# Optimization experiments

Hardware: AMD Instinct MI355X
Metric: run time of the kernel (lower is better)

## Reference

```python
import jax, jax.numpy as jnp
import numpy as np

N = 1000      # dataset / batch samples
D = 2000      # descriptors (e.g., pairwise distances)
A = 200       # atoms
K = 2         # atoms involved per descriptor (distance -> 2)
# nnz = N * D * K * 3 = 12M sparse entries of d_desc/d_pos


def setup_inputs() -> dict:
    key = jax.random.key(0)
    k_val, k_x = jax.random.split(key)
    rng = np.random.default_rng(0)

    # each descriptor involves K atoms (fixed per descriptor, as for distances)
    atoms = rng.integers(0, A, size=(D, K)).astype(np.int32)        # [D, K]

    # expand to per-(sample, descriptor, atom, dim) nonzero entries
    dims = np.arange(3, dtype=np.int32)
    # desc index per nnz within one sample: [D, K, 3] -> flat
    desc_per_sample = np.broadcast_to(np.arange(D, dtype=np.int32)[:, None, None], (D, K, 3)).ravel()
    atom_per_sample = np.broadcast_to(atoms[:, :, None], (D, K, 3)).ravel()
    dim_per_sample = np.broadcast_to(dims[None, None, :], (D, K, 3)).ravel()
    per_sample = D * K * 3

    batch_idx = np.repeat(np.arange(N, dtype=np.int32), per_sample)          # [nnz]
    desc_idx = np.tile(desc_per_sample, N)                                   # [nnz]
    scatter_idx = (batch_idx.astype(np.int64) * (A * 3)
                   + np.tile(atom_per_sample, N).astype(np.int64) * 3
                   + np.tile(dim_per_sample, N)).astype(np.int32)            # [nnz] in [0, N*A*3)

    nnz = N * per_sample
    values = jax.random.normal(k_val, (nnz,), dtype=jnp.float32)             # nonzero d_desc/d_pos
    x = jax.random.normal(k_x, (N, D), dtype=jnp.float32)                    # d_out/d_desc (right input)

    return {
        "values": values,
        "x": x,
        "batch_idx": jnp.asarray(batch_idx),
        "desc_idx": jnp.asarray(desc_idx),
        "scatter_idx": jnp.asarray(scatter_idx),
        "n_atoms": A,
    }


def reference(values, x, batch_idx, desc_idx, scatter_idx, n_atoms):
    # gather right-input entries per nonzero of the sparse left matrix
    right = x[batch_idx, desc_idx]                 # [nnz]
    # per-entry contribution (atom contribution via one descriptor, one dim)
    contrib = right * values                       # [nnz]
    # scatter-add to global d_out/d_pos of shape [N, n_atoms, 3]
    n = x.shape[0]
    out = jax.ops.segment_sum(contrib, scatter_idx, num_segments=n * n_atoms * 3)
    return out.reshape(n, n_atoms, 3)
```

## Files before the change

kernel.cpp:

```cpp
#include <hip/hip_runtime.h>

constexpr int N_SAMPLES  = 1000;
constexpr int D_DESC     = 2000;
constexpr int N_ATOMS    = 200;
constexpr int PER_SAMPLE = 12000;
constexpr int OUT_PER    = 600;
constexpr int N_ENTRIES  = 4000;
constexpr int NH         = 2;
constexpr int EPH        = N_ENTRIES / NH;
constexpr int VPH        = 3 * EPH;
constexpr int XPH        = D_DESC / NH;
constexpr int ELLW_H     = 40;
constexpr int LSENT      = EPH;
constexpr int MTHREADS   = 256;
constexpr int NBLK       = N_SAMPLES * NH;
constexpr int OUT_FLOATS = N_SAMPLES * OUT_PER;
constexpr int OUT_QUADS  = OUT_FLOATS / 4;
constexpr int ZBLKS      = (OUT_QUADS + 255) / 256;
constexpr int ELL_INTS   = NH * N_ATOMS * ELLW_H;
constexpr size_t ELL_BYTES  = (size_t)ELL_INTS * 4;
constexpr size_t PART_BYTES = (size_t)NBLK * OUT_PER * 4;

using f32x4 = __attribute__((ext_vector_type(4))) float;

#define GLD4(dst, ptr) asm volatile("global_load_dwordx4 %0, %1, off" \
    : "=v"(dst) : "v"((unsigned long long)(uintptr_t)(ptr)))

__global__ __launch_bounds__(512)
void setup_kernel(const int* __restrict__ scatter_idx,
                  int* __restrict__ ell,
                  float* __restrict__ out, int zero_out) {
    const int tid = threadIdx.x;
    if (blockIdx.x >= 2) {
        const int i = (blockIdx.x - 2) * 512 + tid;
        if (zero_out && i < OUT_QUADS)
            reinterpret_cast<float4*>(out)[i] = float4{0.f, 0.f, 0.f, 0.f};
        return;
    }
    const int h = blockIdx.x;
    __shared__ int fill[N_ATOMS];
    if (tid < N_ATOMS) fill[tid] = 0;

    int4* ell4 = reinterpret_cast<int4*>(ell + h * N_ATOMS * ELLW_H);
    const int4 sent4 = int4{LSENT, LSENT, LSENT, LSENT};
    for (int i = tid; i < N_ATOMS * ELLW_H / 4; i += 512) ell4[i] = sent4;

    int av[4];
    #pragma unroll
    for (int k = 0; k < 4; ++k) {
        const int le = tid + 512 * k;
        av[k] = (le < EPH) ? (scatter_idx[3 * (h * EPH + le)] / 3) : -1;
    }
    __syncthreads();
    int* ellh = ell + h * N_ATOMS * ELLW_H;
    #pragma unroll
    for (int k = 0; k < 4; ++k) {
        const int le = tid + 512 * k;
        if (av[k] >= 0) {
            const int idx = atomicAdd(&fill[av[k]], 1);
            if (idx < ELLW_H) ellh[av[k] * ELLW_H + idx] = le;
        }
    }
}

template <int MODE>
__global__ __launch_bounds__(MTHREADS)
void SmartDerivatives_kernel(const float* __restrict__ values,
                             const float* __restrict__ x,
                             const int*   __restrict__ ell,
                             float*       __restrict__ pbuf,
                             float*       __restrict__ out) {
    __shared__ __align__(16) float vls[VPH + 4];
    __shared__ __align__(16) float xls[XPH + 4];
    const int bid  = blockIdx.x;
    const int n    = bid >> 1;
    const int h    = bid & 1;
    const int tid  = threadIdx.x;

    const float4* __restrict__ vq = reinterpret_cast<const float4*>(
        values + (size_t)n * PER_SAMPLE + h * VPH);
    const float4* __restrict__ xq = reinterpret_cast<const float4*>(
        x + (size_t)n * D_DESC + h * XPH);

    const int a = (tid < N_ATOMS) ? tid : 0;
    const int4* __restrict__ er =
        reinterpret_cast<const int4*>(ell + ((size_t)h * N_ATOMS + a) * ELLW_H);
    const int4 e0 = er[0], e1 = er[1], e2 = er[2], e3 = er[3], e4 = er[4];

    const int q5 = (tid + 1280 < VPH / 4) ? tid + 1280 : VPH / 4 - 1;
    const int qx = (tid < XPH / 4) ? tid : XPH / 4 - 1;
    f32x4 r0, r1, r2, r3, r4, r5, r6;
    GLD4(r0, vq + tid);
    GLD4(r1, vq + tid + 256);
    GLD4(r2, vq + tid + 512);
    GLD4(r3, vq + tid + 768);
    GLD4(r4, vq + tid + 1024);
    GLD4(r5, vq + q5);
    GLD4(r6, xq + qx);
    asm volatile("s_waitcnt vmcnt(0)");
    __builtin_amdgcn_sched_barrier(0);
    float4* vls4 = reinterpret_cast<float4*>(vls);
    float4* xls4 = reinterpret_cast<float4*>(xls);
    vls4[tid]        = *(const float4*)&r0;
    vls4[tid + 256]  = *(const float4*)&r1;
    vls4[tid + 512]  = *(const float4*)&r2;
    vls4[tid + 768]  = *(const float4*)&r3;
    vls4[tid + 1024] = *(const float4*)&r4;
    vls4[q5]         = *(const float4*)&r5;
    xls4[qx]         = *(const float4*)&r6;
    if (tid < 4)             vls[VPH + tid] = 0.0f;
    if (tid >= 4 && tid < 8) xls[XPH + tid - 4] = 0.0f;

    __syncthreads();

    if (tid < N_ATOMS) {
        float s0 = 0.f, s1 = 0.f, s2 = 0.f;
        #define ACC1(E) { const float xv = xls[(E) >> 1];            \
                          const int   b3 = 3 * (E);                  \
                          s0 += vls[b3 + 0] * xv;                    \
                          s1 += vls[b3 + 1] * xv;                    \
                          s2 += vls[b3 + 2] * xv; }
        #define ACC8(A,B) { ACC1(A.x) ACC1(A.y) ACC1(A.z) ACC1(A.w) \
                            ACC1(B.x) ACC1(B.y) ACC1(B.z) ACC1(B.w) }
        ACC8(e0, e1)
        if (e1.w != LSENT) {
            ACC8(e2, e3)
            if (e3.w != LSENT) {
                ACC1(e4.x) ACC1(e4.y) ACC1(e4.z) ACC1(e4.w)
                if (e4.w != LSENT) {
                    const int4 e5 = er[5], e6 = er[6], e7 = er[7],
                               e8 = er[8], e9 = er[9];
                    ACC8(e5, e6)
                    if (e6.w != LSENT) {
                        ACC8(e7, e8)
                        if (e8.w != LSENT) { ACC1(e9.x) ACC1(e9.y)
                                             ACC1(e9.z) ACC1(e9.w) }
                    }
                }
            }
        }
        #undef ACC8
        #undef ACC1
        if (MODE == 0) {
            float* __restrict__ p = pbuf + (size_t)bid * OUT_PER + 3 * tid;
            p[0] = s0; p[1] = s1; p[2] = s2;
        } else {
            float* __restrict__ o = out + (size_t)n * OUT_PER + 3 * tid;
            unsafeAtomicAdd(o + 0, s0);
            unsafeAtomicAdd(o + 1, s1);
            unsafeAtomicAdd(o + 2, s2);
        }
    }
}

__global__ __launch_bounds__(256)
void reduce_kernel(const float* __restrict__ pbuf, float* __restrict__ out) {
    const int i = blockIdx.x * 256 + threadIdx.x;
    if (i < OUT_QUADS) {
        const int nn = i / 150;
        const int r  = i - nn * 150;
        const float4* __restrict__ p4 = reinterpret_cast<const float4*>(pbuf);
        const float4 A = p4[(size_t)nn * 300 + r];
        const float4 B = p4[(size_t)nn * 300 + 150 + r];
        reinterpret_cast<float4*>(out)[i] =
            float4{A.x + B.x, A.y + B.y, A.z + B.z, A.w + B.w};
    }
}

extern "C" void kernel_launch(void* const* d_in, const int* in_sizes, int n_in,
                              void* d_out, int out_size, void* d_ws, size_t ws_size,
                              hipStream_t stream) {
    const float* values      = (const float*)d_in[0];
    const float* x           = (const float*)d_in[1];
    const int*   scatter_idx = (const int*)d_in[4];
    float*       out         = (float*)d_out;

    int*   ell  = (int*)d_ws;
    float* pbuf = (float*)((char*)d_ws + ELL_BYTES);
    const bool direct = ws_size >= ELL_BYTES + PART_BYTES;

    if (direct) {
        setup_kernel<<<2, 512, 0, stream>>>(scatter_idx, ell, out, 0);
        SmartDerivatives_kernel<0><<<NBLK, MTHREADS, 0, stream>>>(
            values, x, ell, pbuf, out);
        reduce_kernel<<<ZBLKS, 256, 0, stream>>>(pbuf, out);
    } else {
        const int zb = (OUT_QUADS + 511) / 512;
        setup_kernel<<<2 + zb, 512, 0, stream>>>(scatter_idx, ell, out, 1);
        SmartDerivatives_kernel<1><<<NBLK, MTHREADS, 0, stream>>>(
            values, x, ell, pbuf, out);
    }
}
```

Baseline: 24.07 us.

## Premultiply values by x at staging and sort atom rows by entry count

```diff
diff --git a/kernel.cpp b/kernel.cpp
--- a/kernel.cpp
+++ b/kernel.cpp
@@ -19,6 +19,7 @@
 constexpr int ZBLKS      = (OUT_QUADS + 255) / 256;
 constexpr int ELL_INTS   = NH * N_ATOMS * ELLW_H;
 constexpr size_t ELL_BYTES  = (size_t)ELL_INTS * 4;
+constexpr size_t AROW_BYTES = (size_t)NH * N_ATOMS * 4;
 constexpr size_t PART_BYTES = (size_t)NBLK * OUT_PER * 4;
 
 using f32x4 = __attribute__((ext_vector_type(4))) float;
@@ -28,7 +29,7 @@
 
 __global__ __launch_bounds__(512)
 void setup_kernel(const int* __restrict__ scatter_idx,
-                  int* __restrict__ ell,
+                  int* __restrict__ ell, int* __restrict__ arow,
                   float* __restrict__ out, int zero_out) {
     const int tid = threadIdx.x;
     if (blockIdx.x >= 2) {
@@ -38,8 +39,10 @@
         return;
     }
     const int h = blockIdx.x;
-    __shared__ int fill[N_ATOMS];
-    if (tid < N_ATOMS) fill[tid] = 0;
+    __shared__ int cnt[N_ATOMS], fill[N_ATOMS], rankOf[N_ATOMS];
+    __shared__ int hist[ELLW_H + 1], off[ELLW_H + 1];
+    if (tid < N_ATOMS) { cnt[tid] = 0; fill[tid] = 0; }
+    if (tid <= ELLW_H) hist[tid] = 0;
 
     int4* ell4 = reinterpret_cast<int4*>(ell + h * N_ATOMS * ELLW_H);
     const int4 sent4 = int4{LSENT, LSENT, LSENT, LSENT};
@@ -52,13 +55,30 @@
         av[k] = (le < EPH) ? (scatter_idx[3 * (h * EPH + le)] / 3) : -1;
     }
     __syncthreads();
+    #pragma unroll
+    for (int k = 0; k < 4; ++k) if (av[k] >= 0) atomicAdd(&cnt[av[k]], 1);
+    __syncthreads();
+    if (tid < N_ATOMS) atomicAdd(&hist[min(cnt[tid], ELLW_H)], 1);
+    __syncthreads();
+    if (tid == 0) {
+        int run = 0;
+        for (int l = ELLW_H; l >= 0; --l) { off[l] = run; run += hist[l]; }
+    }
+    __syncthreads();
+    if (tid < N_ATOMS) {
+        const int r = atomicAdd(&off[min(cnt[tid], ELLW_H)], 1);
+        rankOf[tid] = r;
+        arow[h * N_ATOMS + r] = tid;
+    }
+    __syncthreads();
     int* ellh = ell + h * N_ATOMS * ELLW_H;
     #pragma unroll
     for (int k = 0; k < 4; ++k) {
         const int le = tid + 512 * k;
         if (av[k] >= 0) {
-            const int idx = atomicAdd(&fill[av[k]], 1);
-            if (idx < ELLW_H) ellh[av[k] * ELLW_H + idx] = le;
+            const int row = rankOf[av[k]];
+            const int idx = atomicAdd(&fill[row], 1);
+            if (idx < ELLW_H) ellh[row * ELLW_H + idx] = le;
         }
     }
 }
@@ -68,58 +88,65 @@
 void SmartDerivatives_kernel(const float* __restrict__ values,
                              const float* __restrict__ x,
                              const int*   __restrict__ ell,
+                             const int*   __restrict__ arow,
                              float*       __restrict__ pbuf,
                              float*       __restrict__ out) {
     __shared__ __align__(16) float vls[VPH + 4];
-    __shared__ __align__(16) float xls[XPH + 4];
-    const int bid  = blockIdx.x;
-    const int n    = bid >> 1;
-    const int h    = bid & 1;
-    const int tid  = threadIdx.x;
+    const int bid = blockIdx.x;
+    const int n   = bid >> 1;
+    const int h   = bid & 1;
+    const int tid = threadIdx.x;
 
     const float4* __restrict__ vq = reinterpret_cast<const float4*>(
         values + (size_t)n * PER_SAMPLE + h * VPH);
-    const float4* __restrict__ xq = reinterpret_cast<const float4*>(
-        x + (size_t)n * D_DESC + h * XPH);
-
-    const int a = (tid < N_ATOMS) ? tid : 0;
+    const float* __restrict__ xg = x + (size_t)n * D_DESC + h * XPH;
+
+    const int row = (tid < N_ATOMS) ? tid : 0;
     const int4* __restrict__ er =
-        reinterpret_cast<const int4*>(ell + ((size_t)h * N_ATOMS + a) * ELLW_H);
+        reinterpret_cast<const int4*>(ell + ((size_t)h * N_ATOMS + row) * ELLW_H);
     const int4 e0 = er[0], e1 = er[1], e2 = er[2], e3 = er[3], e4 = er[4];
-
-    const int q5 = (tid + 1280 < VPH / 4) ? tid + 1280 : VPH / 4 - 1;
-    const int qx = (tid < XPH / 4) ? tid : XPH / 4 - 1;
-    f32x4 r0, r1, r2, r3, r4, r5, r6;
-    GLD4(r0, vq + tid);
-    GLD4(r1, vq + tid + 256);
-    GLD4(r2, vq + tid + 512);
-    GLD4(r3, vq + tid + 768);
-    GLD4(r4, vq + tid + 1024);
-    GLD4(r5, vq + q5);
-    GLD4(r6, xq + qx);
+    const int aout = arow[h * N_ATOMS + row];
+
+    const int q[6] = { tid, tid + 256, tid + 512, tid + 768, tid + 1024,
+                       (tid + 1280 < VPH / 4) ? tid + 1280 : VPH / 4 - 1 };
+    f32x4 r0, r1, r2, r3, r4, r5;
+    GLD4(r0, vq + q[0]); GLD4(r1, vq + q[1]); GLD4(r2, vq + q[2]);
+    GLD4(r3, vq + q[3]); GLD4(r4, vq + q[4]); GLD4(r5, vq + q[5]);
+
+    int   elo[6];
+    float xa[6], xb[6];
+    #pragma unroll
+    for (int s = 0; s < 6; ++s) {
+        const int f0 = 4 * q[s];
+        elo[s] = f0 / 3;
+        xa[s]  = xg[(f0 / 3) >> 1];
+        xb[s]  = xg[((f0 + 3) / 3) >> 1];
+    }
     asm volatile("s_waitcnt vmcnt(0)");
     __builtin_amdgcn_sched_barrier(0);
+
     float4* vls4 = reinterpret_cast<float4*>(vls);
-    float4* xls4 = reinterpret_cast<float4*>(xls);
-    vls4[tid]        = *(const float4*)&r0;
-    vls4[tid + 256]  = *(const float4*)&r1;
-    vls4[tid + 512]  = *(const float4*)&r2;
-    vls4[tid + 768]  = *(const float4*)&r3;
-    vls4[tid + 1024] = *(const float4*)&r4;
-    vls4[q5]         = *(const float4*)&r5;
-    xls4[qx]         = *(const float4*)&r6;
-    if (tid < 4)             vls[VPH + tid] = 0.0f;
-    if (tid >= 4 && tid < 8) xls[XPH + tid - 4] = 0.0f;
+    #define STORE_PROD(S, R) {                                              \
+        const int f0 = 4 * q[S];                                            \
+        float4 p;                                                           \
+        p.x = R[0] * (((f0 + 0) / 3 == elo[S]) ? xa[S] : xb[S]);            \
+        p.y = R[1] * (((f0 + 1) / 3 == elo[S]) ? xa[S] : xb[S]);            \
+        p.z = R[2] * (((f0 + 2) / 3 == elo[S]) ? xa[S] : xb[S]);            \
+        p.w = R[3] * (((f0 + 3) / 3 == elo[S]) ? xa[S] : xb[S]);            \
+        vls4[q[S]] = p; }
+    STORE_PROD(0, r0) STORE_PROD(1, r1) STORE_PROD(2, r2)
+    STORE_PROD(3, r3) STORE_PROD(4, r4) STORE_PROD(5, r5)
+    #undef STORE_PROD
+    if (tid < 4) vls[VPH + tid] = 0.0f;
 
     __syncthreads();
 
     if (tid < N_ATOMS) {
         float s0 = 0.f, s1 = 0.f, s2 = 0.f;
-        #define ACC1(E) { const float xv = xls[(E) >> 1];            \
-                          const int   b3 = 3 * (E);                  \
-                          s0 += vls[b3 + 0] * xv;                    \
-                          s1 += vls[b3 + 1] * xv;                    \
-                          s2 += vls[b3 + 2] * xv; }
+        #define ACC1(E) { const int b3 = 3 * (E);                    \
+                          s0 += vls[b3 + 0];                         \
+                          s1 += vls[b3 + 1];                         \
+                          s2 += vls[b3 + 2]; }
         #define ACC8(A,B) { ACC1(A.x) ACC1(A.y) ACC1(A.z) ACC1(A.w) \
                             ACC1(B.x) ACC1(B.y) ACC1(B.z) ACC1(B.w) }
         ACC8(e0, e1)
@@ -142,10 +169,10 @@
         #undef ACC8
         #undef ACC1
         if (MODE == 0) {
-            float* __restrict__ p = pbuf + (size_t)bid * OUT_PER + 3 * tid;
+            float* __restrict__ p = pbuf + (size_t)bid * OUT_PER + 3 * aout;
             p[0] = s0; p[1] = s1; p[2] = s2;
         } else {
-            float* __restrict__ o = out + (size_t)n * OUT_PER + 3 * tid;
+            float* __restrict__ o = out + (size_t)n * OUT_PER + 3 * aout;
             unsafeAtomicAdd(o + 0, s0);
             unsafeAtomicAdd(o + 1, s1);
             unsafeAtomicAdd(o + 2, s2);
@@ -176,18 +203,19 @@
     float*       out         = (float*)d_out;
 
     int*   ell  = (int*)d_ws;
-    float* pbuf = (float*)((char*)d_ws + ELL_BYTES);
-    const bool direct = ws_size >= ELL_BYTES + PART_BYTES;
+    int*   arow = (int*)((char*)d_ws + ELL_BYTES);
+    float* pbuf = (float*)((char*)d_ws + ELL_BYTES + AROW_BYTES);
+    const bool direct = ws_size >= ELL_BYTES + AROW_BYTES + PART_BYTES;
 
     if (direct) {
-        setup_kernel<<<2, 512, 0, stream>>>(scatter_idx, ell, out, 0);
+        setup_kernel<<<2, 512, 0, stream>>>(scatter_idx, ell, arow, out, 0);
         SmartDerivatives_kernel<0><<<NBLK, MTHREADS, 0, stream>>>(
-            values, x, ell, pbuf, out);
+            values, x, ell, arow, pbuf, out);
         reduce_kernel<<<ZBLKS, 256, 0, stream>>>(pbuf, out);
     } else {
         const int zb = (OUT_QUADS + 511) / 512;
-        setup_kernel<<<2 + zb, 512, 0, stream>>>(scatter_idx, ell, out, 1);
+        setup_kernel<<<2 + zb, 512, 0, stream>>>(scatter_idx, ell, arow, out, 1);
         SmartDerivatives_kernel<1><<<NBLK, MTHREADS, 0, stream>>>(
-            values, x, ell, pbuf, out);
-    }
-}
+            values, x, ell, arow, pbuf, out);
+    }
+}
```

After: 24.23 us. About the same (+0.6%).
